# Kernel tuning notes

Hardware: AMD Instinct MI355X
Metric: run time of the kernel (lower is better)

Reference implementation:

```python
import jax, jax.numpy as jnp
import numpy as np

B, S, D, H, FF, R, NB = 8, 1024, 768, 12, 3072, 16, 768


def _ln(x, g, b, eps=1e-6):
    m = x.mean(-1, keepdims=True)
    v = jnp.mean((x - m) ** 2, axis=-1, keepdims=True)
    return (x - m) * jax.lax.rsqrt(v + eps) * g + b


def setup_inputs() -> dict:
    key = jax.random.key(0)

    def rn(i, shape, s=0.02):
        return jax.random.normal(jax.random.fold_in(key, i), shape, jnp.float32) * s

    inp = {
        "x": jax.random.normal(jax.random.fold_in(key, 0), (B, S, D), jnp.float32),
        "attn_mask": jnp.zeros((S, S), jnp.float32),
        "norm1_g": jnp.ones((D,), jnp.float32),
        "norm1_b": jnp.zeros((D,), jnp.float32),
        "q_w": rn(1, (D, D)), "q_b": jnp.zeros((D,), jnp.float32),
        "k_w": rn(2, (D, D)), "k_b": jnp.zeros((D,), jnp.float32),
        "v_w": rn(3, (D, D)), "v_b": jnp.zeros((D,), jnp.float32),
        "o_w": rn(4, (D, D)), "o_b": jnp.zeros((D,), jnp.float32),
        "norm2_g": jnp.ones((D,), jnp.float32),
        "norm2_b": jnp.zeros((D,), jnp.float32),
        "fc1_w": rn(5, (FF, D)), "fc1_b": jnp.zeros((FF,), jnp.float32),
        "fc2_w": rn(6, (D, FF)), "fc2_b": jnp.zeros((D,), jnp.float32),
        # shared LoRA (backbone tokens)
        "lora1_A": rn(7, (D, R)), "lora1_B": rn(8, (R, FF)),
        "lora2_A": rn(9, (FF, R)), "lora2_B": rn(10, (R, D)),
        # expert VeRA: frozen shared A/B, per-expert diagonal scaling vectors
        "vera1_A": rn(11, (D, R)), "vera1_B": rn(12, (R, FF)),
        "vera2_A": rn(13, (FF, R)), "vera2_B": rn(14, (R, D)),
        "expert_fc1_d": rn(15, (R,), 1.0), "expert_fc1_b": rn(16, (FF,), 1.0),
        "expert_fc2_d": rn(17, (R,), 1.0), "expert_fc2_b": rn(18, (D,), 1.0),
        "num_backbone_tokens": NB,
    }
    return inp


def reference(x, attn_mask, norm1_g, norm1_b, q_w, q_b, k_w, k_b, v_w, v_b,
              o_w, o_b, norm2_g, norm2_b, fc1_w, fc1_b, fc2_w, fc2_b,
              lora1_A, lora1_B, lora2_A, lora2_B,
              vera1_A, vera1_B, vera2_A, vera2_B,
              expert_fc1_d, expert_fc1_b, expert_fc2_d, expert_fc2_b,
              num_backbone_tokens):
    bsz, seq, dim = x.shape
    hd = dim // H                      # head_dim = 64
    scale = hd ** -0.5
    nb = num_backbone_tokens

    # ---- attention (manual bmm + mask + softmax, eval-mode dropout = identity) ----
    h = _ln(x, norm1_g, norm1_b)
    q = (h @ q_w.T + q_b).reshape(bsz, seq, H, hd)
    k = (h @ k_w.T + k_b).reshape(bsz, seq, H, hd)
    v = (h @ v_w.T + v_b).reshape(bsz, seq, H, hd)
    scores = jnp.einsum('bqhd,bkhd->bhqk', q * scale, k) + attn_mask  # [B,H,S,S]
    probs = jax.nn.softmax(scores, axis=-1)
    ao = jnp.einsum('bhqk,bkhd->bqhd', probs, v).reshape(bsz, seq, dim)
    x = x + (ao @ o_w.T + o_b)

    # ---- MLP with split backbone (shared LoRA) / expert (VeRA) adapters ----
    residual = x
    n2 = _ln(x, norm2_g, norm2_b)
    hid = n2 @ fc1_w.T + fc1_b                                   # [B,S,FF]
    hid_b = hid[:, :nb] + (n2[:, :nb] @ lora1_A) @ lora1_B
    hid_e = hid[:, nb:] + (((n2[:, nb:] @ vera1_A) * expert_fc1_d) @ vera1_B) * expert_fc1_b
    hid = jnp.concatenate([hid_b, hid_e], axis=1)
    hid = jax.nn.gelu(hid)
    out = hid @ fc2_w.T + fc2_b                                  # [B,S,D]
    out_b = out[:, :nb] + (hid[:, :nb] @ lora2_A) @ lora2_B
    out_e = out[:, nb:] + (((hid[:, nb:] @ vera2_A) * expert_fc2_d) @ vera2_B) * expert_fc2_b
    out = jnp.concatenate([out_b, out_e], axis=1)
    return residual + out
```

## Files before the change

### kernel.cpp

```cpp
#include <hip/hip_runtime.h>
#include <stdint.h>

#define B_  8
#define S_  1024
#define D_  768
#define H_  12
#define HD_ 64
#define FF_ 3072
#define M_  (B_*S_)
#define R_  16
#define QLD 2304
#define KBLK 128

typedef unsigned short u16;
typedef short s16x8 __attribute__((ext_vector_type(8)));
typedef float fx4  __attribute__((ext_vector_type(4)));

__device__ __forceinline__ float b2f(u16 u) {
  union { unsigned int i; float f; } c; c.i = ((unsigned int)u) << 16; return c.f;
}
__device__ __forceinline__ u16 f2b(float f) {
  union { float f; unsigned int i; } c; c.f = f;
  unsigned int x = c.i;
  x += 0x7FFFu + ((x >> 16) & 1u);
  return (u16)(x >> 16);
}
__device__ __forceinline__ float gelu_f(float x) {
  float u = 0.7978845608028654f * (x + 0.044715f * x * x * x);
  float e = __expf(2.f * u);
  float t = 1.f - 2.f / (e + 1.f);
  return 0.5f * x * (1.f + t);
}
__device__ __forceinline__ void gload16(const u16* gsrc, u16* ldst) {
  __builtin_amdgcn_global_load_lds(
      (__attribute__((address_space(1))) void*)(gsrc),
      (__attribute__((address_space(3))) void*)(ldst), 16, 0, 0);
}

__global__ __launch_bounds__(256)
void cvt_all(const float* __restrict__ q_w, const float* __restrict__ k_w,
             const float* __restrict__ v_w, const float* __restrict__ o_w,
             const float* __restrict__ fc1_w, const float* __restrict__ fc2_w,
             u16* __restrict__ wqkv, u16* __restrict__ wo,
             u16* __restrict__ wfc1, u16* __restrict__ wfc2)
{
  const int i = blockIdx.x * 256 + threadIdx.x;
  const int q1  = D_ * D_ / 4;
  const int fd4 = FF_ * D_ / 4;
  const float* s; u16* d; int j;
  if      (i <     q1)       { s = q_w;   d = wqkv;            j = i; }
  else if (i < 2 * q1)       { s = k_w;   d = wqkv + D_*D_;    j = i - q1; }
  else if (i < 3 * q1)       { s = v_w;   d = wqkv + 2*D_*D_;  j = i - 2*q1; }
  else if (i < 4 * q1)       { s = o_w;   d = wo;              j = i - 3*q1; }
  else if (i < 4 * q1 + fd4) { s = fc1_w; d = wfc1;            j = i - 4*q1; }
  else                       { s = fc2_w; d = wfc2;            j = i - 4*q1 - fd4; }
  const float4 f = ((const float4*)s)[j];
  ushort4 o4; o4.x = f2b(f.x); o4.y = f2b(f.y); o4.z = f2b(f.z); o4.w = f2b(f.w);
  ((ushort4*)d)[j] = o4;
}

__global__ __launch_bounds__(256)
void prep_all(const float* __restrict__ q_bv, const float* __restrict__ k_bv,
              const float* __restrict__ v_bv, float* __restrict__ qkvb,
              const float* __restrict__ lora1B, const float* __restrict__ vera1B,
              const float* __restrict__ e1b, u16* __restrict__ up1L, u16* __restrict__ up1V,
              const float* __restrict__ lora2B, const float* __restrict__ vera2B,
              const float* __restrict__ e2b, u16* __restrict__ up2L, u16* __restrict__ up2V,
              const float* __restrict__ lora2A, const float* __restrict__ vera2A,
              u16* __restrict__ a2tL, u16* __restrict__ a2tV)
{
  const int f = blockIdx.x * 256 + threadIdx.x;
  if (f < QLD)
    qkvb[f] = (f < D_) ? q_bv[f] : (f < 2 * D_) ? k_bv[f - D_] : v_bv[f - 2 * D_];
  {
    const float ev = e1b[f];
    #pragma unroll
    for (int r = 0; r < 16; ++r) {
      up1L[(size_t)f * 32 + r] = f2b(lora1B[(size_t)r * FF_ + f]);
      up1V[(size_t)f * 32 + r] = f2b(vera1B[(size_t)r * FF_ + f] * ev);
      up1L[(size_t)f * 32 + 16 + r] = 0;
      up1V[(size_t)f * 32 + 16 + r] = 0;
    }
  }
  {
    const float4* apl = (const float4*)(lora2A + (size_t)f * 16);
    const float4* apv = (const float4*)(vera2A + (size_t)f * 16);
    #pragma unroll
    for (int q4 = 0; q4 < 4; ++q4) {
      const float4 l4 = apl[q4], v4 = apv[q4];
      a2tL[(size_t)(q4*4+0) * FF_ + f] = f2b(l4.x);
      a2tL[(size_t)(q4*4+1) * FF_ + f] = f2b(l4.y);
      a2tL[(size_t)(q4*4+2) * FF_ + f] = f2b(l4.z);
      a2tL[(size_t)(q4*4+3) * FF_ + f] = f2b(l4.w);
      a2tV[(size_t)(q4*4+0) * FF_ + f] = f2b(v4.x);
      a2tV[(size_t)(q4*4+1) * FF_ + f] = f2b(v4.y);
      a2tV[(size_t)(q4*4+2) * FF_ + f] = f2b(v4.z);
      a2tV[(size_t)(q4*4+3) * FF_ + f] = f2b(v4.w);
    }
  }
  if (f < D_) {
    const float ev = e2b[f];
    #pragma unroll
    for (int r = 0; r < 16; ++r) {
      up2L[(size_t)f * 32 + r] = f2b(lora2B[(size_t)r * D_ + f]);
      up2V[(size_t)f * 32 + r] = f2b(vera2B[(size_t)r * D_ + f] * ev);
      up2L[(size_t)f * 32 + 16 + r] = 0;
      up2V[(size_t)f * 32 + 16 + r] = 0;
    }
  }
}

template<bool ADD>
__global__ __launch_bounds__(256)
void ln_k(const float* __restrict__ x, const u16* __restrict__ add,
          const float* __restrict__ g, const float* __restrict__ beta,
          u16* __restrict__ outb, float* __restrict__ xsum,
          const float* __restrict__ Alora, const float* __restrict__ Avera,
          const float* __restrict__ dvec, u16* __restrict__ tmp1b,
          const int* __restrict__ nbp)
{
  const int row = blockIdx.x;
  const size_t base = (size_t)row * D_;
  float v0[3]; float s = 0.f, sq = 0.f;
  #pragma unroll
  for (int i = 0; i < 3; ++i) {
    const int d = threadIdx.x + i * 256;
    float val = x[base + d];
    if (ADD) { val += b2f(add[base + d]); xsum[base + d] = val; }
    v0[i] = val; s += val; sq += val * val;
  }
  #pragma unroll
  for (int mm = 32; mm >= 1; mm >>= 1) { s += __shfl_xor(s, mm); sq += __shfl_xor(sq, mm); }
  __shared__ float ss[4], s2[4];
  if ((threadIdx.x & 63) == 0) { ss[threadIdx.x >> 6] = s; s2[threadIdx.x >> 6] = sq; }
  __syncthreads();
  s  = ss[0] + ss[1] + ss[2] + ss[3];
  sq = s2[0] + s2[1] + s2[2] + s2[3];
  const float mean = s * (1.f / D_);
  const float var  = sq * (1.f / D_) - mean * mean;
  const float rs   = rsqrtf(var + 1e-6f);
  float nv[3];
  #pragma unroll
  for (int i = 0; i < 3; ++i) {
    const int d = threadIdx.x + i * 256;
    nv[i] = (v0[i] - mean) * rs * g[d] + beta[d];
    outb[base + d] = f2b(nv[i]);
  }

  if (ADD) {
    const int nb = *nbp;
    const bool ex = (row % S_) >= nb;
    const float* Am = ex ? Avera : Alora;
    float p[16];
    #pragma unroll
    for (int r = 0; r < 16; ++r) p[r] = 0.f;
    #pragma unroll
    for (int i = 0; i < 3; ++i) {
      const int d = threadIdx.x + i * 256;
      const float4* ap = (const float4*)(Am + (size_t)d * R_);
      const float4 a0 = ap[0], a1 = ap[1], a2 = ap[2], a3 = ap[3];
      const float vv = nv[i];
      p[0]  += vv * a0.x; p[1]  += vv * a0.y; p[2]  += vv * a0.z; p[3]  += vv * a0.w;
      p[4]  += vv * a1.x; p[5]  += vv * a1.y; p[6]  += vv * a1.z; p[7]  += vv * a1.w;
      p[8]  += vv * a2.x; p[9]  += vv * a2.y; p[10] += vv * a2.z; p[11] += vv * a2.w;
      p[12] += vv * a3.x; p[13] += vv * a3.y; p[14] += vv * a3.z; p[15] += vv * a3.w;
    }
    #pragma unroll
    for (int st = 1; st < 16; st <<= 1)
      #pragma unroll
      for (int r = 0; r < 16; ++r) p[r] += __shfl_xor(p[r], st);
    __shared__ float sred[16][16];
    const int grp = threadIdx.x >> 4;
    if ((threadIdx.x & 15) == 0) {
      #pragma unroll
      for (int r = 0; r < 16; ++r) sred[grp][r] = p[r];
    }
    __syncthreads();
    if (threadIdx.x < 16) {
      float v = 0.f;
      #pragma unroll
      for (int gg = 0; gg < 16; ++gg) v += sred[gg][threadIdx.x];
      if (ex) v *= dvec[threadIdx.x];
      tmp1b[(size_t)row * 32 + threadIdx.x] = f2b(v);
      tmp1b[(size_t)row * 32 + 16 + threadIdx.x] = 0;
    }
  }
}

template<int MODE>
__global__ __launch_bounds__(256)
void gemm_bt(const u16* __restrict__ A, const u16* __restrict__ W,
             const float* __restrict__ bias, u16* __restrict__ Cb,
             float* __restrict__ Cf, const float* __restrict__ resid,
             const u16* __restrict__ Aad, const u16* __restrict__ BadL,
             const u16* __restrict__ BadV, const int* __restrict__ nbp,
             int M, int N, int K)
{
  __shared__ u16 As[128 * 32];
  __shared__ u16 Bs[128 * 32];
  const int tid   = threadIdx.x;
  const int lane  = tid & 63;
  const int wid   = tid >> 6;
  const int wr    = wid >> 1;
  const int wc    = wid & 1;
  const int lr    = lane & 15;
  const int lk    = (lane >> 4) << 3;
  const int m0    = blockIdx.x * 128;
  const int n0    = blockIdx.y * 128;
  const int kg    = (tid & 3) * 8;
  const int row_a = tid >> 2;

  fx4 acc[4][4];
  const fx4 zero = {0.f, 0.f, 0.f, 0.f};
  #pragma unroll
  for (int i = 0; i < 4; ++i)
    #pragma unroll
    for (int j = 0; j < 4; ++j) acc[i][j] = zero;

  for (int k0 = 0; k0 < K; k0 += 32) {
    #pragma unroll
    for (int u = 0; u < 2; ++u) {
      const int row = u * 64 + row_a;
      const int li  = u * 256 + tid;
      gload16(A + (size_t)(m0 + row) * K + k0 + kg, &As[li * 8]);
      gload16(W + (size_t)(n0 + row) * K + k0 + kg, &Bs[li * 8]);
    }
    __syncthreads();
    s16x8 av[4], bv[4];
    #pragma unroll
    for (int i = 0; i < 4; ++i)
      av[i] = *(const s16x8*)&As[(wr * 64 + i * 16 + lr) * 32 + lk];
    #pragma unroll
    for (int j = 0; j < 4; ++j)
      bv[j] = *(const s16x8*)&Bs[(wc * 64 + j * 16 + lr) * 32 + lk];
    #pragma unroll
    for (int i = 0; i < 4; ++i)
      #pragma unroll
      for (int j = 0; j < 4; ++j)
        acc[i][j] = __builtin_amdgcn_mfma_f32_16x16x32_bf16(av[i], bv[j], acc[i][j], 0, 0, 0);
    __syncthreads();
  }

  if (MODE >= 1) {
    const int nb = *nbp;
    const u16* Bad = ((m0 % S_) >= nb) ? BadV : BadL;
    #pragma unroll
    for (int u = 0; u < 2; ++u) {
      const int row = u * 64 + row_a;
      const int li  = u * 256 + tid;
      gload16(Aad + (size_t)(m0 + row) * 32 + kg, &As[li * 8]);
      gload16(Bad + (size_t)(n0 + row) * 32 + kg, &Bs[li * 8]);
    }
    __syncthreads();
    s16x8 av[4], bv[4];
    #pragma unroll
    for (int i = 0; i < 4; ++i)
      av[i] = *(const s16x8*)&As[(wr * 64 + i * 16 + lr) * 32 + lk];
    #pragma unroll
    for (int j = 0; j < 4; ++j)
      bv[j] = *(const s16x8*)&Bs[(wc * 64 + j * 16 + lr) * 32 + lk];
    #pragma unroll
    for (int i = 0; i < 4; ++i)
      #pragma unroll
      for (int j = 0; j < 4; ++j)
        acc[i][j] = __builtin_amdgcn_mfma_f32_16x16x32_bf16(av[i], bv[j], acc[i][j], 0, 0, 0);
    __syncthreads();
  }

  const int rb = (lane >> 4) * 4;
  #pragma unroll
  for (int j = 0; j < 4; ++j) {
    const int col = n0 + wc * 64 + j * 16 + lr;
    const float bj = bias ? bias[col] : 0.f;
    #pragma unroll
    for (int i = 0; i < 4; ++i) {
      const int row = m0 + wr * 64 + i * 16 + rb;
      #pragma unroll
      for (int r = 0; r < 4; ++r) {
        const float val = acc[i][j][r] + bj;
        const size_t idx = (size_t)(row + r) * N + col;
        if (MODE == 1)      Cb[idx] = f2b(gelu_f(val));
        else if (MODE == 2) Cf[idx] = resid[idx] + val;
        else                Cb[idx] = f2b(val);
      }
    }
  }
}

__global__ __launch_bounds__(256)
void downproj(const u16* __restrict__ hid, const u16* __restrict__ A2tL,
              const u16* __restrict__ A2tV, float* __restrict__ part,
              const int* __restrict__ nbp)
{
  __shared__ u16 As[128 * 32];
  __shared__ u16 Bs[16 * 32];
  const int tid  = threadIdx.x;
  const int lane = tid & 63;
  const int w    = tid >> 6;
  const int lr   = lane & 15;
  const int lk   = (lane >> 4) << 3;
  const int m0   = blockIdx.x * 128;
  const int kb   = blockIdx.y * (FF_ / 8);
  const int nb   = *nbp;
  const u16* A2t = ((m0 % S_) >= nb) ? A2tV : A2tL;
  const int kg    = (tid & 3) * 8;
  const int row_a = tid >> 2;

  const fx4 zero = {0.f, 0.f, 0.f, 0.f};
  fx4 acc[2]; acc[0] = zero; acc[1] = zero;

  for (int k0 = kb; k0 < kb + FF_ / 8; k0 += 32) {
    #pragma unroll
    for (int u = 0; u < 2; ++u)
      gload16(hid + (size_t)(m0 + u * 64 + row_a) * FF_ + k0 + kg,
              &As[(u * 256 + tid) * 8]);
    if (tid < 64)
      gload16(A2t + (size_t)(tid >> 2) * FF_ + k0 + kg, &Bs[tid * 8]);
    __syncthreads();
    s16x8 bv = *(const s16x8*)&Bs[lr * 32 + lk];
    #pragma unroll
    for (int i = 0; i < 2; ++i) {
      s16x8 av = *(const s16x8*)&As[(w * 32 + i * 16 + lr) * 32 + lk];
      acc[i] = __builtin_amdgcn_mfma_f32_16x16x32_bf16(av, bv, acc[i], 0, 0, 0);
    }
    __syncthreads();
  }

  const int rb = (lane >> 4) * 4;
  #pragma unroll
  for (int i = 0; i < 2; ++i)
    #pragma unroll
    for (int r = 0; r < 4; ++r)
      part[(size_t)blockIdx.y * M_ * 16 +
           (size_t)(m0 + w * 32 + i * 16 + rb + r) * 16 + lr] = acc[i][r];
}

__global__ __launch_bounds__(256)
void reduce_dp(const float* __restrict__ part, const float* __restrict__ d2,
               u16* __restrict__ tmp2b, const int* __restrict__ nbp)
{
  const int idx = blockIdx.x * 256 + threadIdx.x;
  const int m = idx >> 4, r = idx & 15;
  const int nb = *nbp;
  float s = 0.f;
  #pragma unroll
  for (int ks = 0; ks < 8; ++ks) s += part[(size_t)ks * M_ * 16 + idx];
  if ((m % S_) >= nb) s *= d2[r];
  tmp2b[(size_t)m * 32 + r] = f2b(s);
  tmp2b[(size_t)m * 32 + 16 + r] = 0;
}

__global__ __launch_bounds__(256)
void attn_mfma(const u16* __restrict__ qkv, const float* __restrict__ mask,
               u16* __restrict__ o)
{
  __shared__ u16 Kl[128 * 64];
  __shared__ u16 Vt[64 * 128];
  __shared__ u16 QP[4 * 2048];

  const int tid  = threadIdx.x;
  const int lane = tid & 63;
  const int wq   = tid >> 6;
  const int lr   = lane & 15;
  const int hi   = lane >> 4;
  const int qb   = blockIdx.x;
  const int bh   = blockIdx.y;
  const int b    = bh / H_;
  const int h    = bh % H_;
  const size_t tok0 = (size_t)b * S_ + (size_t)qb * 64;
  const size_t colh = (size_t)h * HD_;

  #pragma unroll
  for (int u = 0; u < 2; ++u) {
    const int li = u * 256 + tid;
    const int r  = li >> 3;
    const int cb = ((li & 7) ^ (r & 7)) * 8;
    gload16(qkv + (tok0 + r) * QLD + colh + cb, &QP[li * 8]);
  }
  __syncthreads();
  s16x8 qa[2];
  {
    const int qrow = wq * 16 + lr;
    #pragma unroll
    for (int ks = 0; ks < 2; ++ks)
      qa[ks] = *(const s16x8*)&QP[qrow * 64 + ((ks * 32 + hi * 8) ^ ((qrow & 7) << 3))];
  }

  const fx4 zero = {0.f, 0.f, 0.f, 0.f};
  fx4 oacc[4];
  #pragma unroll
  for (int dj = 0; dj < 4; ++dj) oacc[dj] = zero;
  float mreg[4], lreg[4];
  #pragma unroll
  for (int r = 0; r < 4; ++r) { mreg[r] = -3.0e38f; lreg[r] = 0.f; }

  for (int kt = 0; kt < S_ / KBLK; ++kt) {
    const size_t ktok = (size_t)b * S_ + (size_t)kt * KBLK;
    __syncthreads();

    #pragma unroll
    for (int u = 0; u < 4; ++u) {
      const int li = u * 256 + tid;
      const int r  = li >> 3;
      const int cb = ((li & 7) ^ (r & 7)) * 8;
      gload16(qkv + (ktok + r) * QLD + D_ + colh + cb, &Kl[li * 8]);
    }
    {
      const int a  = tid >> 3;
      const int c8 = (tid & 7) * 8;
      const u16* vp = qkv + (ktok + 4 * a) * QLD + 2 * D_ + colh + c8;
      s16x8 v0 = *(const s16x8*)vp;
      s16x8 v1 = *(const s16x8*)(vp + QLD);
      s16x8 v2 = *(const s16x8*)(vp + 2 * QLD);
      s16x8 v3 = *(const s16x8*)(vp + 3 * QLD);
      #pragma unroll
      for (int jj = 0; jj < 8; ++jj) {
        const int d  = c8 + jj;
        const int sw = ((d & 7) ^ ((d >> 3) & 7)) << 3;
        const int cp = (4 * a) ^ sw;
        *(uint32_t*)&Vt[d * 128 + cp] =
            (uint32_t)(u16)v0[jj] | ((uint32_t)(u16)v1[jj] << 16);
        *(uint32_t*)&Vt[d * 128 + cp + 2] =
            (uint32_t)(u16)v2[jj] | ((uint32_t)(u16)v3[jj] << 16);
      }
    }
    __syncthreads();

    float val[8][4];
    #pragma unroll
    for (int jh = 0; jh < 2; ++jh) {
      s16x8 kb2[4][2];
      #pragma unroll
      for (int j = 0; j < 4; ++j) {
        const int n = (jh * 4 + j) * 16 + lr;
        #pragma unroll
        for (int ks = 0; ks < 2; ++ks)
          kb2[j][ks] = *(const s16x8*)&Kl[n * 64 + ((ks * 32 + hi * 8) ^ ((n & 7) << 3))];
      }
      float mvh[4][4];
      {
        const float* mp = mask + (size_t)(qb * 64 + wq * 16 + hi * 4) * S_
                        + (size_t)kt * KBLK + jh * 64 + lr;
        #pragma unroll
        for (int j = 0; j < 4; ++j)
          #pragma unroll
          for (int r = 0; r < 4; ++r)
            mvh[j][r] = mp[(size_t)r * S_ + j * 16];
      }
      fx4 sf[4];
      #pragma unroll
      for (int j = 0; j < 4; ++j) sf[j] = zero;
      __builtin_amdgcn_s_setprio(1);
      #pragma unroll
      for (int ks = 0; ks < 2; ++ks)
        #pragma unroll
        for (int j = 0; j < 4; ++j)
          sf[j] = __builtin_amdgcn_mfma_f32_16x16x32_bf16(qa[ks], kb2[j][ks], sf[j], 0, 0, 0);
      __builtin_amdgcn_s_setprio(0);
      #pragma unroll
      for (int j = 0; j < 4; ++j)
        #pragma unroll
        for (int r = 0; r < 4; ++r)
          val[jh * 4 + j][r] = sf[j][r] * 0.125f + mvh[j][r];
    }

    #pragma unroll
    for (int r = 0; r < 4; ++r) {
      float mx = val[0][r];
      #pragma unroll
      for (int j = 1; j < 8; ++j) mx = fmaxf(mx, val[j][r]);
      mx = fmaxf(mx, __shfl_xor(mx, 1));
      mx = fmaxf(mx, __shfl_xor(mx, 2));
      mx = fmaxf(mx, __shfl_xor(mx, 4));
      mx = fmaxf(mx, __shfl_xor(mx, 8));
      const float mn  = fmaxf(mreg[r], mx);
      const float fac = __expf(mreg[r] - mn);
      mreg[r] = mn;
      float rs = 0.f;
      #pragma unroll
      for (int j = 0; j < 8; ++j) {
        const float p = __expf(val[j][r] - mn);
        val[j][r] = p;
        rs += p;
      }
      rs += __shfl_xor(rs, 1); rs += __shfl_xor(rs, 2);
      rs += __shfl_xor(rs, 4); rs += __shfl_xor(rs, 8);
      lreg[r] = lreg[r] * fac + rs;
      #pragma unroll
      for (int dj = 0; dj < 4; ++dj) oacc[dj][r] *= fac;
    }

    #pragma unroll
    for (int j = 0; j < 8; ++j) {
      const int col = j * 16 + lr;
      #pragma unroll
      for (int r = 0; r < 4; ++r) {
        const int row = hi * 4 + r;
        QP[wq * 2048 + row * 128 + (col ^ ((row & 7) << 3))] = f2b(val[j][r]);
      }
    }

    #pragma unroll
    for (int ks = 0; ks < 4; ++ks) {
      s16x8 pa = *(const s16x8*)&QP[wq * 2048 + lr * 128 +
                                    ((ks * 32 + hi * 8) ^ ((lr & 7) << 3))];
      s16x8 bv2[4];
      #pragma unroll
      for (int dj = 0; dj < 4; ++dj) {
        const int n  = dj * 16 + lr;
        const int sw = ((n & 7) ^ ((n >> 3) & 7)) << 3;
        bv2[dj] = *(const s16x8*)&Vt[n * 128 + ((ks * 32 + hi * 8) ^ sw)];
      }
      __builtin_amdgcn_s_setprio(1);
      #pragma unroll
      for (int dj = 0; dj < 4; ++dj)
        oacc[dj] = __builtin_amdgcn_mfma_f32_16x16x32_bf16(pa, bv2[dj], oacc[dj], 0, 0, 0);
      __builtin_amdgcn_s_setprio(0);
    }
  }

  #pragma unroll
  for (int r = 0; r < 4; ++r) {
    const float inv = 1.f / lreg[r];
    const size_t grow = (tok0 + wq * 16 + hi * 4 + r) * D_ + colh;
    #pragma unroll
    for (int dj = 0; dj < 4; ++dj)
      o[grow + dj * 16 + lr] = f2b(oacc[dj][r] * inv);
  }
}

extern "C" void kernel_launch(void* const* d_in, const int* in_sizes, int n_in,
                              void* d_out, int out_size, void* d_ws, size_t ws_size,
                              hipStream_t stream)
{
  const float* x      = (const float*)d_in[0];
  const float* mask   = (const float*)d_in[1];
  const float* n1g    = (const float*)d_in[2];
  const float* n1b    = (const float*)d_in[3];
  const float* q_w    = (const float*)d_in[4];
  const float* q_bv   = (const float*)d_in[5];
  const float* k_w    = (const float*)d_in[6];
  const float* k_bv   = (const float*)d_in[7];
  const float* v_w    = (const float*)d_in[8];
  const float* v_bv   = (const float*)d_in[9];
  const float* o_w    = (const float*)d_in[10];
  const float* o_bv   = (const float*)d_in[11];
  const float* n2g    = (const float*)d_in[12];
  const float* n2b    = (const float*)d_in[13];
  const float* fc1_w  = (const float*)d_in[14];
  const float* fc1_bv = (const float*)d_in[15];
  const float* fc2_w  = (const float*)d_in[16];
  const float* fc2_bv = (const float*)d_in[17];
  const float* lora1A = (const float*)d_in[18];
  const float* lora1B = (const float*)d_in[19];
  const float* lora2A = (const float*)d_in[20];
  const float* lora2B = (const float*)d_in[21];
  const float* vera1A = (const float*)d_in[22];
  const float* vera1B = (const float*)d_in[23];
  const float* vera2A = (const float*)d_in[24];
  const float* vera2B = (const float*)d_in[25];
  const float* e1d    = (const float*)d_in[26];
  const float* e1b    = (const float*)d_in[27];
  const float* e2d    = (const float*)d_in[28];
  const float* e2b    = (const float*)d_in[29];
  const int*   nbp    = (const int*)d_in[30];

  char* wsb = (char*)d_ws;
  u16* h1    = (u16*)wsb; wsb += (size_t)M_ * D_ * 2;
  u16* qkv   = (u16*)wsb; wsb += (size_t)M_ * QLD * 2;
  u16* attno = (u16*)wsb; wsb += (size_t)M_ * D_ * 2;
  u16* oproj = (u16*)wsb; wsb += (size_t)M_ * D_ * 2;
  u16* n2    = (u16*)wsb; wsb += (size_t)M_ * D_ * 2;
  u16* wqkv  = (u16*)wsb; wsb += (size_t)QLD * D_ * 2;
  u16* wo    = (u16*)wsb; wsb += (size_t)D_ * D_ * 2;
  u16* wfc1  = (u16*)wsb; wsb += (size_t)FF_ * D_ * 2;
  u16* wfc2  = (u16*)wsb; wsb += (size_t)D_ * FF_ * 2;
  u16* tmp1b = (u16*)wsb; wsb += (size_t)M_ * 32 * 2;
  u16* tmp2b = (u16*)wsb; wsb += (size_t)M_ * 32 * 2;
  u16* up1L  = (u16*)wsb; wsb += (size_t)FF_ * 32 * 2;
  u16* up1V  = (u16*)wsb; wsb += (size_t)FF_ * 32 * 2;
  u16* up2L  = (u16*)wsb; wsb += (size_t)D_ * 32 * 2;
  u16* up2V  = (u16*)wsb; wsb += (size_t)D_ * 32 * 2;
  u16* a2tL  = (u16*)wsb; wsb += (size_t)16 * FF_ * 2;
  u16* a2tV  = (u16*)wsb; wsb += (size_t)16 * FF_ * 2;
  float* qkvb = (float*)wsb; wsb += (size_t)QLD * 4;
  float* part = (float*)wsb; wsb += (size_t)8 * M_ * 16 * 4;
  u16* hidb = h1;

  const int totq = (4 * D_ * D_ + 2 * FF_ * D_) / 4;
  cvt_all<<<totq / 256, 256, 0, stream>>>(q_w, k_w, v_w, o_w, fc1_w, fc2_w,
                                          wqkv, wo, wfc1, wfc2);
  prep_all<<<FF_ / 256, 256, 0, stream>>>(q_bv, k_bv, v_bv, qkvb,
                                          lora1B, vera1B, e1b, up1L, up1V,
                                          lora2B, vera2B, e2b, up2L, up2V,
                                          lora2A, vera2A, a2tL, a2tV);

  ln_k<false><<<M_, 256, 0, stream>>>(x, nullptr, n1g, n1b, h1, nullptr,
                                      nullptr, nullptr, nullptr, nullptr, nullptr);
  gemm_bt<0><<<dim3(M_/128, QLD/128), 256, 0, stream>>>(
      h1, wqkv, qkvb, qkv, nullptr, nullptr, nullptr, nullptr, nullptr, nullptr,
      M_, QLD, D_);
  attn_mfma<<<dim3(S_/64, B_*H_), 256, 0, stream>>>(qkv, mask, attno);
  gemm_bt<0><<<dim3(M_/128, D_/128), 256, 0, stream>>>(
      attno, wo, o_bv, oproj, nullptr, nullptr, nullptr, nullptr, nullptr, nullptr,
      M_, D_, D_);

  ln_k<true><<<M_, 256, 0, stream>>>(x, oproj, n2g, n2b, n2, (float*)d_out,
                                     lora1A, vera1A, e1d, tmp1b, nbp);

  gemm_bt<1><<<dim3(M_/128, FF_/128), 256, 0, stream>>>(
      n2, wfc1, fc1_bv, hidb, nullptr, nullptr, tmp1b, up1L, up1V, nbp,
      M_, FF_, D_);

  downproj<<<dim3(M_/128, 8), 256, 0, stream>>>(hidb, a2tL, a2tV, part, nbp);
  reduce_dp<<<M_*16/256, 256, 0, stream>>>(part, e2d, tmp2b, nbp);

  gemm_bt<2><<<dim3(M_/128, D_/128), 256, 0, stream>>>(
      hidb, wfc2, fc2_bv, nullptr, (float*)d_out, (const float*)d_out,
      tmp2b, up2L, up2V, nbp, M_, D_, FF_);
}
```

Baseline: 385.8 us.

## Double-buffer K/V tiles in attention and remap blocks across XCDs

The attention kernel now keeps two LDS buffers for K and transposed V. It issues the global loads for the next key tile before computing scores on the current tile, and writes the V transpose into the alternate buffer after the softmax. This removes one barrier per iteration and overlaps global memory latency with MFMA work, at the cost of doubling K/V LDS usage, which may lower occupancy. The grid is also flattened and remapped, using (lin&7)*192, so consecutive blocks on the same XCD share a batch-head, to improve L2 reuse of K/V.

```diff
diff --git a/kernel.cpp b/kernel.cpp
--- a/kernel.cpp
+++ b/kernel.cpp
@@ -354,8 +354,8 @@
 void attn_mfma(const u16* __restrict__ qkv, const float* __restrict__ mask,
                u16* __restrict__ o)
 {
-  __shared__ u16 Kl[128 * 64];
-  __shared__ u16 Vt[64 * 128];
+  __shared__ u16 Kl[2][128 * 64];
+  __shared__ u16 Vt[2][64 * 128];
   __shared__ u16 QP[4 * 2048];
 
   const int tid  = threadIdx.x;
@@ -363,12 +363,17 @@
   const int wq   = tid >> 6;
   const int lr   = lane & 15;
   const int hi   = lane >> 4;
-  const int qb   = blockIdx.x;
-  const int bh   = blockIdx.y;
+  const int lin = blockIdx.x;
+  const int vsw = (lin & 7) * 192 + (lin >> 3);
+  const int qb  = vsw & 15;
+  const int bh  = vsw >> 4;
   const int b    = bh / H_;
   const int h    = bh % H_;
   const size_t tok0 = (size_t)b * S_ + (size_t)qb * 64;
   const size_t colh = (size_t)h * HD_;
+
+  const int va  = tid >> 3;
+  const int vc8 = (tid & 7) * 8;
 
   #pragma unroll
   for (int u = 0; u < 2; ++u) {
@@ -377,54 +382,71 @@
     const int cb = ((li & 7) ^ (r & 7)) * 8;
     gload16(qkv + (tok0 + r) * QLD + colh + cb, &QP[li * 8]);
   }
-  __syncthreads();
-  s16x8 qa[2];
   {
-    const int qrow = wq * 16 + lr;
-    #pragma unroll
-    for (int ks = 0; ks < 2; ++ks)
-      qa[ks] = *(const s16x8*)&QP[qrow * 64 + ((ks * 32 + hi * 8) ^ ((qrow & 7) << 3))];
-  }
-
-  const fx4 zero = {0.f, 0.f, 0.f, 0.f};
-  fx4 oacc[4];
-  #pragma unroll
-  for (int dj = 0; dj < 4; ++dj) oacc[dj] = zero;
-  float mreg[4], lreg[4];
-  #pragma unroll
-  for (int r = 0; r < 4; ++r) { mreg[r] = -3.0e38f; lreg[r] = 0.f; }
-
-  for (int kt = 0; kt < S_ / KBLK; ++kt) {
-    const size_t ktok = (size_t)b * S_ + (size_t)kt * KBLK;
-    __syncthreads();
-
+    const size_t ktok = (size_t)b * S_;
     #pragma unroll
     for (int u = 0; u < 4; ++u) {
       const int li = u * 256 + tid;
       const int r  = li >> 3;
       const int cb = ((li & 7) ^ (r & 7)) * 8;
-      gload16(qkv + (ktok + r) * QLD + D_ + colh + cb, &Kl[li * 8]);
-    }
-    {
-      const int a  = tid >> 3;
-      const int c8 = (tid & 7) * 8;
-      const u16* vp = qkv + (ktok + 4 * a) * QLD + 2 * D_ + colh + c8;
-      s16x8 v0 = *(const s16x8*)vp;
-      s16x8 v1 = *(const s16x8*)(vp + QLD);
-      s16x8 v2 = *(const s16x8*)(vp + 2 * QLD);
-      s16x8 v3 = *(const s16x8*)(vp + 3 * QLD);
-      #pragma unroll
-      for (int jj = 0; jj < 8; ++jj) {
-        const int d  = c8 + jj;
-        const int sw = ((d & 7) ^ ((d >> 3) & 7)) << 3;
-        const int cp = (4 * a) ^ sw;
-        *(uint32_t*)&Vt[d * 128 + cp] =
-            (uint32_t)(u16)v0[jj] | ((uint32_t)(u16)v1[jj] << 16);
-        *(uint32_t*)&Vt[d * 128 + cp + 2] =
-            (uint32_t)(u16)v2[jj] | ((uint32_t)(u16)v3[jj] << 16);
-      }
-    }
-    __syncthreads();
+      gload16(qkv + (ktok + r) * QLD + D_ + colh + cb, &Kl[0][li * 8]);
+    }
+    const u16* vp = qkv + (ktok + 4 * va) * QLD + 2 * D_ + colh + vc8;
+    s16x8 w0 = *(const s16x8*)vp;
+    s16x8 w1 = *(const s16x8*)(vp + QLD);
+    s16x8 w2 = *(const s16x8*)(vp + 2 * QLD);
+    s16x8 w3 = *(const s16x8*)(vp + 3 * QLD);
+    #pragma unroll
+    for (int jj = 0; jj < 8; ++jj) {
+      const int d  = vc8 + jj;
+      const int sw = ((d & 7) ^ ((d >> 3) & 7)) << 3;
+      const int cp = (4 * va) ^ sw;
+      *(uint32_t*)&Vt[0][d * 128 + cp] =
+          (uint32_t)(u16)w0[jj] | ((uint32_t)(u16)w1[jj] << 16);
+      *(uint32_t*)&Vt[0][d * 128 + cp + 2] =
+          (uint32_t)(u16)w2[jj] | ((uint32_t)(u16)w3[jj] << 16);
+    }
+  }
+  __syncthreads();
+
+  s16x8 qa[2];
+  {
+    const int qrow = wq * 16 + lr;
+    #pragma unroll
+    for (int ks = 0; ks < 2; ++ks)
+      qa[ks] = *(const s16x8*)&QP[qrow * 64 + ((ks * 32 + hi * 8) ^ ((qrow & 7) << 3))];
+  }
+  __syncthreads();
+
+  const fx4 zero = {0.f, 0.f, 0.f, 0.f};
+  fx4 oacc[4];
+  #pragma unroll
+  for (int dj = 0; dj < 4; ++dj) oacc[dj] = zero;
+  float mreg[4], lreg[4];
+  #pragma unroll
+  for (int r = 0; r < 4; ++r) { mreg[r] = -3.0e38f; lreg[r] = 0.f; }
+
+  const int NT = S_ / KBLK;
+  for (int kt = 0; kt < NT; ++kt) {
+    const int cur = kt & 1;
+    const int nxt = cur ^ 1;
+
+    s16x8 w0, w1, w2, w3;
+    if (kt + 1 < NT) {
+      const size_t ktokn = (size_t)b * S_ + (size_t)(kt + 1) * KBLK;
+      #pragma unroll
+      for (int u = 0; u < 4; ++u) {
+        const int li = u * 256 + tid;
+        const int r  = li >> 3;
+        const int cb = ((li & 7) ^ (r & 7)) * 8;
+        gload16(qkv + (ktokn + r) * QLD + D_ + colh + cb, &Kl[nxt][li * 8]);
+      }
+      const u16* vp = qkv + (ktokn + 4 * va) * QLD + 2 * D_ + colh + vc8;
+      w0 = *(const s16x8*)vp;
+      w1 = *(const s16x8*)(vp + QLD);
+      w2 = *(const s16x8*)(vp + 2 * QLD);
+      w3 = *(const s16x8*)(vp + 3 * QLD);
+    }
 
     float val[8][4];
     #pragma unroll
@@ -435,7 +457,7 @@
         const int n = (jh * 4 + j) * 16 + lr;
         #pragma unroll
         for (int ks = 0; ks < 2; ++ks)
-          kb2[j][ks] = *(const s16x8*)&Kl[n * 64 + ((ks * 32 + hi * 8) ^ ((n & 7) << 3))];
+          kb2[j][ks] = *(const s16x8*)&Kl[cur][n * 64 + ((ks * 32 + hi * 8) ^ ((n & 7) << 3))];
       }
       float mvh[4][4];
       {
@@ -500,6 +522,19 @@
       }
     }
 
+    if (kt + 1 < NT) {
+      #pragma unroll
+      for (int jj = 0; jj < 8; ++jj) {
+        const int d  = vc8 + jj;
+        const int sw = ((d & 7) ^ ((d >> 3) & 7)) << 3;
+        const int cp = (4 * va) ^ sw;
+        *(uint32_t*)&Vt[nxt][d * 128 + cp] =
+            (uint32_t)(u16)w0[jj] | ((uint32_t)(u16)w1[jj] << 16);
+        *(uint32_t*)&Vt[nxt][d * 128 + cp + 2] =
+            (uint32_t)(u16)w2[jj] | ((uint32_t)(u16)w3[jj] << 16);
+      }
+    }
+
     #pragma unroll
     for (int ks = 0; ks < 4; ++ks) {
       s16x8 pa = *(const s16x8*)&QP[wq * 2048 + lr * 128 +
@@ -509,7 +544,7 @@
       for (int dj = 0; dj < 4; ++dj) {
         const int n  = dj * 16 + lr;
         const int sw = ((n & 7) ^ ((n >> 3) & 7)) << 3;
-        bv2[dj] = *(const s16x8*)&Vt[n * 128 + ((ks * 32 + hi * 8) ^ sw)];
+        bv2[dj] = *(const s16x8*)&Vt[cur][n * 128 + ((ks * 32 + hi * 8) ^ sw)];
       }
       __builtin_amdgcn_s_setprio(1);
       #pragma unroll
@@ -517,6 +552,8 @@
         oacc[dj] = __builtin_amdgcn_mfma_f32_16x16x32_bf16(pa, bv2[dj], oacc[dj], 0, 0, 0);
       __builtin_amdgcn_s_setprio(0);
     }
+
+    __syncthreads();
   }
 
   #pragma unroll
@@ -600,7 +637,7 @@
   gemm_bt<0><<<dim3(M_/128, QLD/128), 256, 0, stream>>>(
       h1, wqkv, qkvb, qkv, nullptr, nullptr, nullptr, nullptr, nullptr, nullptr,
       M_, QLD, D_);
-  attn_mfma<<<dim3(S_/64, B_*H_), 256, 0, stream>>>(qkv, mask, attno);
+  attn_mfma<<<(S_/64) * (B_*H_), 256, 0, stream>>>(qkv, mask, attno);
   gemm_bt<0><<<dim3(M_/128, D_/128), 256, 0, stream>>>(
       attno, wo, o_bv, oproj, nullptr, nullptr, nullptr, nullptr, nullptr, nullptr,
       M_, D_, D_);
```

New measurement: 382.3 us. Within noise of the previous version (-0.9%).
